# Performance work log

Hardware: AMD Instinct MI355X
Metric: run time of the kernel (lower is better)

Reference implementation:

```python
import jax, jax.numpy as jnp
import numpy as np

D_MODEL = 512
N_HEADS = 8
D_K = 64
B, T = 64, 256


def setup_inputs() -> dict:
    key = jax.random.key(0)
    ks = jax.random.split(key, 5)
    x = jax.random.normal(ks[0], (B, T, D_MODEL), dtype=jnp.float32)
    s = 1.0 / np.sqrt(D_MODEL)
    Wq = jax.random.normal(ks[1], (N_HEADS, D_MODEL, D_K), dtype=jnp.float32) * s
    Wk = jax.random.normal(ks[2], (N_HEADS, D_MODEL, D_K), dtype=jnp.float32) * s
    Wv = jax.random.normal(ks[3], (N_HEADS, D_MODEL, D_K), dtype=jnp.float32) * s
    Wo = jax.random.normal(ks[4], (N_HEADS * D_K, D_MODEL), dtype=jnp.float32) * s
    return {"x": x, "Wq": Wq, "Wk": Wk, "Wv": Wv, "Wo": Wo}


def reference(x, Wq, Wk, Wv, Wo):
    Bc, Tc, C = x.shape  # C == d_model; source scales by C**0.5, not sqrt(d_k)
    q = jnp.einsum('btc,hcd->bhtd', x, Wq)
    k = jnp.einsum('btc,hcd->bhtd', x, Wk)
    v = jnp.einsum('btc,hcd->bhtd', x, Wv)
    scores = jnp.einsum('bhtd,bhsd->bhts', q, k) / jnp.sqrt(jnp.float32(C))
    causal = jnp.tril(jnp.ones((Tc, Tc), dtype=bool))
    scores = jnp.where(causal, scores, -jnp.inf)
    attn = jax.nn.softmax(scores, axis=-1)  # dropout = identity in eval mode
    out = jnp.einsum('bhts,bhsd->bhtd', attn, v)
    out = out.transpose(0, 2, 1, 3).reshape(Bc, Tc, -1)  # concat heads
    return out @ Wo  # final dropout = identity in eval mode
```

## Files before the change

kernel.cpp:

```cpp
#include <hip/hip_runtime.h>
#include <hip/hip_bf16.h>

typedef __attribute__((ext_vector_type(4))) float f32x4;
typedef __attribute__((ext_vector_type(8))) short bf16x8;
typedef __attribute__((ext_vector_type(4))) short s16x4;
typedef __attribute__((ext_vector_type(4))) unsigned int u32x4;

#define DEV static __device__ __forceinline__

DEV unsigned short f2b(float f) {
  union { float f; unsigned int u; } v; v.f = f;
  unsigned int u = v.u;
  return (unsigned short)((u + 0x7fffu + ((u >> 16) & 1u)) >> 16);
}

DEV void gll16(const void* g, void* l) {
  __builtin_amdgcn_global_load_lds((__attribute__((address_space(1))) void*)g,
                                   (__attribute__((address_space(3))) void*)l,
                                   16, 0, 0);
}

__global__ __launch_bounds__(256) void prep(const float* __restrict__ x,
                                            const float* __restrict__ Wq,
                                            const float* __restrict__ Wk,
                                            const float* __restrict__ Wv,
                                            const float* __restrict__ Wo,
                                            unsigned short* __restrict__ xb,
                                            unsigned short* __restrict__ Wt,
                                            unsigned short* __restrict__ WoT) {
  int id = blockIdx.x * 256 + threadIdx.x;
  if (id < 2097152) {
    f32x4 v = *(const f32x4*)(x + (long)id * 4);
    s16x4 o;
    o.x = (short)f2b(v.x); o.y = (short)f2b(v.y);
    o.z = (short)f2b(v.z); o.w = (short)f2b(v.w);
    *(s16x4*)(xb + (long)id * 4) = o;
  } else {
    int j = id - 2097152;
    if (j < 786432) {
      int n = j >> 9, c = j & 511;
      int proj = n >> 9, hh = (n >> 6) & 7, d = n & 63;
      const float* W = (proj == 0) ? Wq : ((proj == 1) ? Wk : Wv);
      Wt[j] = f2b(W[hh * 32768 + c * 64 + d]);
    } else {
      int k = j - 786432;
      int n = k >> 9, c = k & 511;
      WoT[k] = f2b(Wo[c * 512 + n]);
    }
  }
}

template <int F32OUT>
__global__ __launch_bounds__(256, 2) void gemm_bt(const unsigned short* __restrict__ A,
                                                  const unsigned short* __restrict__ BT,
                                                  void* __restrict__ Cv,
                                                  int N) {
  const int K = 512;
  __shared__ unsigned short As[128 * 64];
  __shared__ unsigned short Bs[128 * 64];

  const int tid = threadIdx.x;
  const int wave = tid >> 6, lane = tid & 63;
  const int quad = lane >> 4, l16 = lane & 15;
  const int wm = wave >> 1, wn = wave & 1;
  const int bm = blockIdx.x, bn = blockIdx.y;

  const int srow = lane >> 3;
  const int scol = ((lane & 7) ^ srow) * 8;

  f32x4 acc[4][4] = {};

  for (int kk = 0; kk < K; kk += 64) {
    __syncthreads();
#pragma unroll
    for (int s = 0; s < 4; s++) {
      int seg = wave * 4 + s;
      int row = seg * 8 + srow;
      gll16(A + (long)(bm * 128 + row) * K + kk + scol, As + seg * 512);
      gll16(BT + (long)(bn * 128 + row) * K + kk + scol, Bs + seg * 512);
    }
    __syncthreads();

#pragma unroll
    for (int kc = 0; kc < 2; kc++) {
      const int rq = (((kc * 4 + quad) ^ (l16 & 7)) * 8);
      bf16x8 af[4], bfv[4];
#pragma unroll
      for (int mt = 0; mt < 4; mt++)
        af[mt] = *(const bf16x8*)(As + (wm * 64 + mt * 16 + l16) * 64 + rq);
#pragma unroll
      for (int nt = 0; nt < 4; nt++)
        bfv[nt] = *(const bf16x8*)(Bs + (wn * 64 + nt * 16 + l16) * 64 + rq);
#pragma unroll
      for (int mt = 0; mt < 4; mt++)
#pragma unroll
        for (int nt = 0; nt < 4; nt++)
          acc[mt][nt] = __builtin_amdgcn_mfma_f32_16x16x32_bf16(af[mt], bfv[nt], acc[mt][nt], 0, 0, 0);
    }
  }

#pragma unroll
  for (int mt = 0; mt < 4; mt++) {
#pragma unroll
    for (int nt = 0; nt < 4; nt++) {
      int row0 = bm * 128 + wm * 64 + mt * 16 + quad * 4;
      int col = bn * 128 + wn * 64 + nt * 16 + l16;
      if (F32OUT) {
        float* cp = (float*)Cv + (long)row0 * N + col;
#pragma unroll
        for (int r = 0; r < 4; r++)
          cp[(long)r * N] = acc[mt][nt][r];
      } else {
        unsigned short* cp = (unsigned short*)Cv + (long)row0 * N + col;
#pragma unroll
        for (int r = 0; r < 4; r++)
          cp[(long)r * N] = f2b(acc[mt][nt][r]);
      }
    }
  }
}

__global__ __launch_bounds__(256, 2) void attn(const unsigned short* __restrict__ QKV,
                                               unsigned short* __restrict__ AO) {
  const int bh = blockIdx.x;
  const int b = bh >> 3, h = bh & 7;
  const int tid = threadIdx.x;
  const int wave = tid >> 6, lane = tid & 63;
  const int quad = lane >> 4, l16 = lane & 15;

  __shared__ unsigned short Kl[256 * 64];
  __shared__ unsigned short Vt[64 * 264];
  __shared__ unsigned short Pl[4][32 * 40];

  const unsigned short* Qb = QKV + (long)b * 256 * 1536 + h * 64;
  const unsigned short* Kb = Qb + 512;
  const unsigned short* Vb = Qb + 1024;

  {
    int r = lane >> 3, cg = lane & 7;
#pragma unroll
    for (int s = 0; s < 8; s++) {
      int seg = wave * 8 + s;
      gll16(Kb + (long)(seg * 8 + r) * 1536 + ((cg ^ r) * 8), Kl + seg * 512);
    }
  }
  {
    int j = tid;
    const unsigned short* vp = Vb + (long)j * 1536;
#pragma unroll
    for (int g = 0; g < 8; g++) {
      union { u32x4 v; unsigned short s[8]; } d;
      d.v = *(const u32x4*)(vp + g * 8);
#pragma unroll
      for (int q = 0; q < 8; q++)
        Vt[(g * 8 + q) * 264 + j] = d.s[q];
    }
  }
  const int tiles[2] = {wave, 7 - wave};
  bf16x8 qf[2][2][2];
#pragma unroll
  for (int ti = 0; ti < 2; ti++)
#pragma unroll
    for (int kc = 0; kc < 2; kc++)
#pragma unroll
      for (int mt = 0; mt < 2; mt++)
        qf[ti][kc][mt] = *(const bf16x8*)(Qb +
            (long)(tiles[ti] * 32 + mt * 16 + l16) * 1536 + kc * 32 + quad * 8);

  __syncthreads();

  f32x4 O[2][2][4] = {};
  float lsum[2][2][4] = {};
  const float scale = 0.044194173824159216f;

#pragma unroll
  for (int ti = 0; ti < 2; ti++) {
    const int t = tiles[ti];
    for (int c32 = 0; c32 <= t; c32++) {
      f32x4 S[2][2] = {};
#pragma unroll
      for (int kc = 0; kc < 2; kc++) {
        bf16x8 kbf[2];
#pragma unroll
        for (int st = 0; st < 2; st++) {
          int jrow = c32 * 32 + st * 16 + l16;
          kbf[st] = *(const bf16x8*)(Kl + jrow * 64 + (((kc * 4 + quad) ^ (jrow & 7)) * 8));
        }
#pragma unroll
        for (int mt = 0; mt < 2; mt++)
#pragma unroll
          for (int st = 0; st < 2; st++)
            S[mt][st] = __builtin_amdgcn_mfma_f32_16x16x32_bf16(qf[ti][kc][mt], kbf[st], S[mt][st], 0, 0, 0);
      }
      const bool diag = (c32 == t);
#pragma unroll
      for (int mt = 0; mt < 2; mt++)
#pragma unroll
        for (int st = 0; st < 2; st++)
#pragma unroll
          for (int r = 0; r < 4; r++) {
            int trow = mt * 16 + quad * 4 + r;
            float p = __expf(S[mt][st][r] * scale);
            if (diag && (st * 16 + l16 > trow)) p = 0.0f;
            lsum[ti][mt][r] += p;
            Pl[wave][trow * 40 + st * 16 + l16] = f2b(p);
          }
      bf16x8 pa[2], vbf[4];
#pragma unroll
      for (int mt = 0; mt < 2; mt++)
        pa[mt] = *(const bf16x8*)(&Pl[wave][(mt * 16 + l16) * 40 + quad * 8]);
#pragma unroll
      for (int dt = 0; dt < 4; dt++)
        vbf[dt] = *(const bf16x8*)(Vt + (dt * 16 + l16) * 264 + c32 * 32 + quad * 8);
#pragma unroll
      for (int mt = 0; mt < 2; mt++)
#pragma unroll
        for (int dt = 0; dt < 4; dt++)
          O[ti][mt][dt] = __builtin_amdgcn_mfma_f32_16x16x32_bf16(pa[mt], vbf[dt], O[ti][mt][dt], 0, 0, 0);
    }
  }

  float linv[2][2][4];
#pragma unroll
  for (int ti = 0; ti < 2; ti++)
#pragma unroll
    for (int mt = 0; mt < 2; mt++)
#pragma unroll
      for (int r = 0; r < 4; r++) {
        float s = lsum[ti][mt][r];
        s += __shfl_xor(s, 1); s += __shfl_xor(s, 2);
        s += __shfl_xor(s, 4); s += __shfl_xor(s, 8);
        linv[ti][mt][r] = 1.0f / s;
      }
#pragma unroll
  for (int ti = 0; ti < 2; ti++)
#pragma unroll
    for (int mt = 0; mt < 2; mt++)
#pragma unroll
      for (int dt = 0; dt < 4; dt++)
#pragma unroll
        for (int r = 0; r < 4; r++) {
          int t_ = tiles[ti] * 32 + mt * 16 + quad * 4 + r;
          int d = dt * 16 + l16;
          AO[(long)(b * 256 + t_) * 512 + h * 64 + d] = f2b(O[ti][mt][dt][r] * linv[ti][mt][r]);
        }
}

extern "C" void kernel_launch(void* const* d_in, const int* in_sizes, int n_in,
                              void* d_out, int out_size, void* d_ws, size_t ws_size,
                              hipStream_t stream) {
  const float* x  = (const float*)d_in[0];
  const float* Wq = (const float*)d_in[1];
  const float* Wk = (const float*)d_in[2];
  const float* Wv = (const float*)d_in[3];
  const float* Wo = (const float*)d_in[4];

  unsigned short* Wt  = (unsigned short*)d_ws;
  unsigned short* WoT = Wt + 1536 * 512;
  unsigned short* xb  = WoT + 512 * 512;
  unsigned short* QKV = xb + (long)16384 * 512;
  unsigned short* AO  = QKV + (long)16384 * 1536;
  float* out = (float*)d_out;

  prep<<<12288, 256, 0, stream>>>(x, Wq, Wk, Wv, Wo, xb, Wt, WoT);

  dim3 g1(128, 12);
  gemm_bt<0><<<g1, 256, 0, stream>>>(xb, Wt, (void*)QKV, 1536);

  attn<<<512, 256, 0, stream>>>(QKV, AO);

  dim3 g2(128, 4);
  gemm_bt<1><<<g2, 256, 0, stream>>>(AO, WoT, (void*)out, 512);
}
```

Measured before the change: 164.7 us.

## Tile weight transposes through LDS and remap GEMM blocks per XCD

After: 156.7 us. -4.9%, faster.

```diff
diff --git a/kernel.cpp b/kernel.cpp
--- a/kernel.cpp
+++ b/kernel.cpp
@@ -28,24 +28,52 @@
                                             unsigned short* __restrict__ xb,
                                             unsigned short* __restrict__ Wt,
                                             unsigned short* __restrict__ WoT) {
-  int id = blockIdx.x * 256 + threadIdx.x;
-  if (id < 2097152) {
+  const int bid = blockIdx.x;
+  if (bid < 8192) {
+    int id = bid * 256 + threadIdx.x;
     f32x4 v = *(const f32x4*)(x + (long)id * 4);
     s16x4 o;
     o.x = (short)f2b(v.x); o.y = (short)f2b(v.y);
     o.z = (short)f2b(v.z); o.w = (short)f2b(v.w);
     *(s16x4*)(xb + (long)id * 4) = o;
+    return;
+  }
+
+  __shared__ unsigned int L[64 * 65];
+  const int tx = threadIdx.x & 63;
+  const int ty = threadIdx.x >> 6;
+
+  int tb = bid - 8192;
+  if (tb < 192) {
+    int proj = tb >> 6, h = (tb >> 3) & 7, c0 = (tb & 7) << 6;
+    const float* W = (proj == 0) ? Wq : ((proj == 1) ? Wk : Wv);
+    const float* base = W + (long)h * 32768 + (long)c0 * 64;
+#pragma unroll
+    for (int i = 0; i < 16; i++) {
+      int c = ty + i * 4;
+      L[tx * 65 + c] = f2b(base[(long)c * 64 + tx]);
+    }
+    __syncthreads();
+    unsigned short* out = Wt + ((long)(proj * 512 + h * 64)) * 512 + c0;
+#pragma unroll
+    for (int i = 0; i < 16; i++) {
+      int d = ty + i * 4;
+      out[(long)d * 512 + tx] = (unsigned short)L[d * 65 + tx];
+    }
   } else {
-    int j = id - 2097152;
-    if (j < 786432) {
-      int n = j >> 9, c = j & 511;
-      int proj = n >> 9, hh = (n >> 6) & 7, d = n & 63;
-      const float* W = (proj == 0) ? Wq : ((proj == 1) ? Wk : Wv);
-      Wt[j] = f2b(W[hh * 32768 + c * 64 + d]);
-    } else {
-      int k = j - 786432;
-      int n = k >> 9, c = k & 511;
-      WoT[k] = f2b(Wo[c * 512 + n]);
+    int t = tb - 192;
+    int n0 = (t >> 3) << 6, c0 = (t & 7) << 6;
+#pragma unroll
+    for (int i = 0; i < 16; i++) {
+      int c = ty + i * 4;
+      L[tx * 65 + c] = f2b(Wo[(long)(c0 + c) * 512 + n0 + tx]);
+    }
+    __syncthreads();
+    unsigned short* out = WoT + (long)n0 * 512 + c0;
+#pragma unroll
+    for (int i = 0; i < 16; i++) {
+      int n = ty + i * 4;
+      out[(long)n * 512 + tx] = (unsigned short)L[n * 65 + tx];
     }
   }
 }
@@ -63,7 +91,14 @@
   const int wave = tid >> 6, lane = tid & 63;
   const int quad = lane >> 4, l16 = lane & 15;
   const int wm = wave >> 1, wn = wave & 1;
-  const int bm = blockIdx.x, bn = blockIdx.y;
+
+  const int NB = N >> 7;
+  const int nwg = gridDim.x;
+  const int q = nwg >> 3, r = nwg & 7;
+  const int xcd = blockIdx.x & 7, ci = blockIdx.x >> 3;
+  const int wg = (xcd < r ? xcd * (q + 1) : r * (q + 1) + (xcd - r) * q) + ci;
+  const int bn = wg % NB;
+  const int bm = wg / NB;
 
   const int srow = lane >> 3;
   const int scol = ((lane & 7) ^ srow) * 8;
@@ -108,13 +143,13 @@
       if (F32OUT) {
         float* cp = (float*)Cv + (long)row0 * N + col;
 #pragma unroll
-        for (int r = 0; r < 4; r++)
-          cp[(long)r * N] = acc[mt][nt][r];
+        for (int r2 = 0; r2 < 4; r2++)
+          cp[(long)r2 * N] = acc[mt][nt][r2];
       } else {
         unsigned short* cp = (unsigned short*)Cv + (long)row0 * N + col;
 #pragma unroll
-        for (int r = 0; r < 4; r++)
-          cp[(long)r * N] = f2b(acc[mt][nt][r]);
+        for (int r2 = 0; r2 < 4; r2++)
+          cp[(long)r2 * N] = f2b(acc[mt][nt][r2]);
       }
     }
   }
@@ -262,13 +297,11 @@
   unsigned short* AO  = QKV + (long)16384 * 1536;
   float* out = (float*)d_out;
 
-  prep<<<12288, 256, 0, stream>>>(x, Wq, Wk, Wv, Wo, xb, Wt, WoT);
-
-  dim3 g1(128, 12);
-  gemm_bt<0><<<g1, 256, 0, stream>>>(xb, Wt, (void*)QKV, 1536);
+  prep<<<8448, 256, 0, stream>>>(x, Wq, Wk, Wv, Wo, xb, Wt, WoT);
+
+  gemm_bt<0><<<1536, 256, 0, stream>>>(xb, Wt, (void*)QKV, 1536);
 
   attn<<<512, 256, 0, stream>>>(QKV, AO);
 
-  dim3 g2(128, 4);
-  gemm_bt<1><<<g2, 256, 0, stream>>>(AO, WoT, (void*)out, 512);
-}
+  gemm_bt<1><<<512, 256, 0, stream>>>(AO, WoT, (void*)out, 512);
+}
```
